# Optimization experiments

Hardware: AMD Instinct MI355X
Metric: run time of the kernel (lower is better)

## Reference

```python
import math
import jax, jax.numpy as jnp
import numpy as np

IN_CH = 512
OUT_CH = 512
KSIZE = 3
STYLE_DIM = 512
EPS = 1e-8


def setup_inputs() -> dict:
    key = jax.random.key(0)
    ks = jax.random.split(key, 8)
    B, H, W = 16, 32, 32
    x = jax.random.normal(ks[0], (B, IN_CH, H, W), dtype=jnp.float32)
    style = jax.random.normal(ks[1], (B, STYLE_DIM), dtype=jnp.float32)
    noise = jax.random.normal(ks[2], (B, 1, 2 * H, 2 * W), dtype=jnp.float32)
    # learned params (matching torch init semantics)
    conv_weight = jax.random.normal(ks[3], (OUT_CH, IN_CH, KSIZE, KSIZE), dtype=jnp.float32)
    mod_weight = jax.random.normal(ks[4], (IN_CH, STYLE_DIM), dtype=jnp.float32)
    mod_bias = jnp.ones((IN_CH,), dtype=jnp.float32)  # bias_init=1
    noise_weight = jax.random.normal(ks[5], (1,), dtype=jnp.float32) * 0.1
    act_bias = jnp.zeros((OUT_CH,), dtype=jnp.float32)
    return {"x": x, "style": style, "noise": noise, "conv_weight": conv_weight,
            "mod_weight": mod_weight, "mod_bias": mod_bias,
            "noise_weight": noise_weight, "act_bias": act_bias}


def _blur_kernel_2d():
    k = jnp.array([1.0, 3.0, 3.0, 1.0], dtype=jnp.float32)
    k2 = k[None, :] * k[:, None]
    k2 = k2 / k2.sum()
    return k2 * 4.0  # upsample_factor**2


def _styled_conv_up(x, style, conv_weight, mod_weight, mod_bias,
                    noise_weight, act_bias, noise):
    B, C_in, H, W = x.shape
    # EqualLinear modulation: scale = 1/sqrt(style_dim), lr_mul=1
    s = style @ (mod_weight * (1.0 / math.sqrt(STYLE_DIM))).T + mod_bias  # [B, C_in]
    # modulate + demodulate per-sample weights
    wscale = 1.0 / math.sqrt(C_in * KSIZE * KSIZE)
    w = wscale * conv_weight[None] * s[:, None, :, None, None]  # [B, out, in, k, k]
    demod = jax.lax.rsqrt(jnp.sum(w * w, axis=(2, 3, 4)) + EPS)  # [B, out]
    w = w * demod[:, :, None, None, None]
    # conv_transpose2d(stride=2, padding=0) == lhs_dilated conv with spatially
    # flipped kernel. torch passes weight as (in, out, k, k); equivalent OIHW
    # forward kernel is flip(w) with layout (out, in, k, k).
    w_flip = jnp.flip(w, axis=(-2, -1))

    def single(xi, wi):  # xi [in,H,W], wi [out,in,k,k]
        return jax.lax.conv_general_dilated(
            xi[None], wi, window_strides=(1, 1),
            padding=[(KSIZE - 1, KSIZE - 1)] * 2,
            lhs_dilation=(2, 2),
            dimension_numbers=("NCHW", "OIHW", "NCHW"))[0]

    out = jax.vmap(single)(x, w_flip)  # [B, out, 2H+1, 2W+1] for k=3
    # Blur: upfirdn2d(kernel=4x4, pad=(1,1)) -> depthwise valid conv
    Bc, Co, Ho, Wo = out.shape
    kb = _blur_kernel_2d()[None, None]  # [1,1,4,4] (symmetric, flip is a no-op)
    out = jax.lax.conv_general_dilated(
        out.reshape(Bc * Co, 1, Ho, Wo), kb, window_strides=(1, 1),
        padding=[(1, 1), (1, 1)],
        dimension_numbers=("NCHW", "OIHW", "NCHW"))
    out = out.reshape(Bc, Co, Ho + 2 - 3, Wo + 2 - 3)  # [B, out, 2H, 2W]
    # noise injection + FusedLeakyReLU (slope 0.2, scale sqrt(2))
    out = out + noise_weight * noise
    out = jax.nn.leaky_relu(out + act_bias.reshape(1, -1, 1, 1), 0.2) * math.sqrt(2.0)
    return out


def reference(x, style, noise, conv_weight, mod_weight, mod_bias,
              noise_weight, act_bias):
    return _styled_conv_up(x, style, conv_weight, mod_weight, mod_bias,
                           noise_weight, act_bias, noise)
```

## Files before the change

### kernel.cpp

```cpp
#include <hip/hip_runtime.h>
#include <math.h>


typedef __attribute__((ext_vector_type(8))) __bf16 bf16x8;
typedef __attribute__((ext_vector_type(4))) float f32x4;

#define WSCALE 0.014731391274719739f
#define SSCALE 0.044194173824159216f

__device__ __forceinline__ unsigned short f2bf(float f) {
  unsigned u = __builtin_bit_cast(unsigned, f);
  u += 0x7fff + ((u >> 16) & 1);
  return (unsigned short)(u >> 16);
}
__device__ __forceinline__ float bf2f(unsigned short h) {
  unsigned u = ((unsigned)h) << 16;
  return __builtin_bit_cast(float, u);
}

__global__ __launch_bounds__(256) void k_style(
    const float* __restrict__ style, const float* __restrict__ mod_w,
    const float* __restrict__ mod_b, float* __restrict__ s_out) {
  int wid  = (blockIdx.x * 256 + threadIdx.x) >> 6;
  int lane = threadIdx.x & 63;
  int b = wid >> 9, ic = wid & 511;
  float acc = 0.f;
  for (int j = lane; j < 512; j += 64)
    acc += style[b * 512 + j] * mod_w[ic * 512 + j];
  for (int off = 32; off > 0; off >>= 1) acc += __shfl_down(acc, off);
  if (lane == 0) s_out[b * 512 + ic] = acc * SSCALE + mod_b[ic];
}

__device__ const int SLABTAP[9] = {0, 2, 6, 8, 1, 7, 3, 5, 4};
__device__ const int SLABOFF[4] = {0, 4, 6, 8};
__device__ const int TAPN[4]    = {4, 2, 2, 1};
__device__ const int TOFFp[4][4] = {{0,-1,-34,-35},{0,-34,0,0},{0,-1,0,0},{0,0,0,0}};

__global__ __launch_bounds__(256) void k_w2(
    const float* __restrict__ conv_w, unsigned short* __restrict__ W2,
    float* __restrict__ w2s) {
  __shared__ float t[4608];
  const int oc = blockIdx.x;
  for (int i = threadIdx.x; i < 4608; i += 256) t[i] = conv_w[oc * 4608 + i];
  __syncthreads();
  for (int i = threadIdx.x; i < 4608; i += 256) {
    int tg = i >> 9, ic = i & 511;
    W2[((size_t)(tg * 512 + oc)) * 512 + ic] = f2bf(t[ic * 9 + SLABTAP[tg]]);
  }
  for (int i = threadIdx.x; i < 512; i += 256) {
    float a = 0.f;
    #pragma unroll
    for (int tg = 0; tg < 9; tg++) { float w = t[i * 9 + tg]; a += w * w; }
    w2s[oc * 512 + i] = a;
  }
}

__global__ __launch_bounds__(256) void k_demod(
    const float* __restrict__ w2s, const float* __restrict__ s,
    float* __restrict__ dscale) {
  int wid  = (blockIdx.x * 256 + threadIdx.x) >> 6;
  int lane = threadIdx.x & 63;
  int b = wid >> 9, oc = wid & 511;
  float acc = 0.f;
  for (int ic = lane; ic < 512; ic += 64) {
    float sv = s[b * 512 + ic];
    acc += sv * sv * w2s[oc * 512 + ic];
  }
  for (int off = 32; off > 0; off >>= 1) acc += __shfl_down(acc, off);
  if (lane == 0)
    dscale[b * 512 + oc] = WSCALE * rsqrtf(WSCALE * WSCALE * acc + 1e-8f);
}

__global__ __launch_bounds__(256) void k_xs2(
    const float* __restrict__ x, const float* __restrict__ s,
    unsigned short* __restrict__ S2) {
  __shared__ float xt[64][65];
  const int b = blockIdx.z, ic0 = blockIdx.y * 64, r0 = blockIdx.x * 2;
  for (int i = threadIdx.x; i < 4096; i += 256) {
    int icL = i >> 6, pxL = i & 63;
    int gr = r0 + (pxL >> 5), gc = pxL & 31;
    xt[icL][pxL] = x[((b * 512 + ic0 + icL) * 32 + gr) * 32 + gc] * s[b * 512 + ic0 + icL];
  }
  __syncthreads();
  for (int i = threadIdx.x; i < 512; i += 256) {
    int pxL = i >> 3, icO = i & 7;
    unsigned short tmp[8];
    #pragma unroll
    for (int k = 0; k < 8; k++) tmp[k] = f2bf(xt[icO * 8 + k][pxL]);
    int gr = r0 + (pxL >> 5), gc = pxL & 31;
    int R = (gr + 1) * 34 + (gc + 1);
    *(uint4*)(&S2[((size_t)b * 1156 + R) * 512 + ic0 + icO * 8]) = *(const uint4*)tmp;
  }
}

__global__ void k_zero(unsigned short* __restrict__ S2) {
  int b = blockIdx.y, id = blockIdx.x;
  int ry, rx;
  if (id < 34)       { ry = 0;        rx = id; }
  else if (id < 68)  { ry = 33;       rx = id - 34; }
  else if (id < 100) { ry = id - 67;  rx = 0; }
  else               { ry = id - 99;  rx = 33; }
  ((unsigned*)(S2 + ((size_t)b * 1156 + ry * 34 + rx) * 512))[threadIdx.x] = 0;
}

__global__ __launch_bounds__(256, 2) void k_gemm(
    const unsigned short* __restrict__ S2, const unsigned short* __restrict__ W2,
    const float* __restrict__ dscale, unsigned short* __restrict__ I, int b_base) {
  __shared__ __align__(16) unsigned short As[128][64];
  __shared__ __align__(16) unsigned short Bs[256][64];

  const int nblk = gridDim.x, qq = nblk >> 3, lid = blockIdx.x;
  const int swz = (lid & 7) * qq + (lid >> 3);
  const int bl = swz / 80;  int rr = swz - bl * 80;
  const int p  = rr / 20;   rr -= p * 20;
  const int nt = rr >> 2, mt = rr & 3;
  const int b  = b_base + bl;
  const int m0 = mt * 128, n0 = nt * 256;

  const int tid = threadIdx.x, lane = tid & 63;
  const int wv = tid >> 6, wm = wv >> 1, wn = wv & 1;
  const int l15 = lane & 15, quad = lane >> 4;
  const int ntap = TAPN[p], soff = SLABOFF[p];
  const int kq = tid & 7, rw = tid >> 3;

  int gRow[8];
  #pragma unroll
  for (int it = 0; it < 8; it++) {
    int n = n0 + it * 32 + rw;
    if (n < 1089) {
      int uy = n / 33, ux = n - uy * 33;
      gRow[it] = b * 1156 + (uy + 1) * 34 + (ux + 1);
    } else gRow[it] = -1;
  }

  f32x4 acc[4][8];
  #pragma unroll
  for (int m = 0; m < 4; m++)
    #pragma unroll
    for (int n = 0; n < 8; n++) acc[m][n] = (f32x4)0.f;

  const int kend = ntap * 512;

  uint4 ra[4], rb[8];
  {
    const int off0 = TOFFp[p][0];
    #pragma unroll
    for (int it = 0; it < 4; it++)
      ra[it] = *(const uint4*)(W2 + ((size_t)(soff * 512 + m0 + it * 32 + rw)) * 512 + kq * 8);
    #pragma unroll
    for (int it = 0; it < 8; it++) {
      uint4 v = make_uint4(0u, 0u, 0u, 0u);
      if (gRow[it] >= 0)
        v = *(const uint4*)(S2 + (size_t)(gRow[it] + off0) * 512 + kq * 8);
      rb[it] = v;
    }
  }

  #pragma unroll 1
  for (int k0 = 0; k0 < kend; k0 += 64) {
    __syncthreads();
    #pragma unroll
    for (int it = 0; it < 4; it++) {
      int r = it * 32 + rw;
      *(uint4*)(&As[r][(kq ^ (r & 7)) * 8]) = ra[it];
    }
    #pragma unroll
    for (int it = 0; it < 8; it++) {
      int r = it * 32 + rw;
      *(uint4*)(&Bs[r][(kq ^ (r & 7)) * 8]) = rb[it];
    }
    const int k1 = k0 + 64;
    if (k1 < kend) {
      const int tj1   = k1 >> 9;
      const int icw1  = k1 & 511;
      const int off1  = TOFFp[p][tj1];
      const int slab1 = soff + tj1;
      #pragma unroll
      for (int it = 0; it < 4; it++)
        ra[it] = *(const uint4*)(W2 + ((size_t)(slab1 * 512 + m0 + it * 32 + rw)) * 512 + icw1 + kq * 8);
      #pragma unroll
      for (int it = 0; it < 8; it++) {
        uint4 v = make_uint4(0u, 0u, 0u, 0u);
        if (gRow[it] >= 0)
          v = *(const uint4*)(S2 + (size_t)(gRow[it] + off1) * 512 + icw1 + kq * 8);
        rb[it] = v;
      }
    }
    __syncthreads();
    #pragma unroll
    for (int kk = 0; kk < 2; kk++) {
      bf16x8 af[4], bfr[8];
      #pragma unroll
      for (int m = 0; m < 4; m++) {
        int r = wm * 64 + m * 16 + l15;
        af[m] = *(const bf16x8*)(&As[r][((kk * 4 + quad) ^ (r & 7)) * 8]);
      }
      #pragma unroll
      for (int n = 0; n < 8; n++) {
        int r = wn * 128 + n * 16 + l15;
        bfr[n] = *(const bf16x8*)(&Bs[r][((kk * 4 + quad) ^ (r & 7)) * 8]);
      }
      #pragma unroll
      for (int m = 0; m < 4; m++)
        #pragma unroll
        for (int n = 0; n < 8; n++)
          acc[m][n] = __builtin_amdgcn_mfma_f32_16x16x32_bf16(af[m], bfr[n], acc[m][n], 0, 0, 0);
    }
  }

  float dsv[4][4];
  #pragma unroll
  for (int m = 0; m < 4; m++)
    #pragma unroll
    for (int r = 0; r < 4; r++)
      dsv[m][r] = dscale[b * 512 + m0 + wm * 64 + m * 16 + quad * 4 + r];
  const size_t Ibase = ((size_t)(bl * 4 + p) * 512) * 1096;
  #pragma unroll
  for (int n = 0; n < 8; n++) {
    int nf = n0 + wn * 128 + n * 16 + l15;
    if (nf < 1089) {
      #pragma unroll
      for (int m = 0; m < 4; m++) {
        int oc = m0 + wm * 64 + m * 16 + quad * 4;
        #pragma unroll
        for (int r = 0; r < 4; r++)
          I[Ibase + (size_t)(oc + r) * 1096 + nf] = f2bf(acc[m][n][r] * dsv[m][r]);
      }
    }
  }
}

__global__ __launch_bounds__(256) void k_blur(
    const unsigned short* __restrict__ I, const float* __restrict__ noise,
    const float* __restrict__ noise_w, const float* __restrict__ act_b,
    float* __restrict__ out, int b_base) {
  __shared__ __align__(16) unsigned short Ism[4][1096];
  __shared__ float V[64][67];
  const int oc = blockIdx.x, bl = blockIdx.y, b = b_base + bl;
  for (int i = threadIdx.x; i < 548; i += 256) {
    int p = i / 137, w = i - p * 137;
    *(uint4*)(&Ism[p][w * 8]) =
        *(const uint4*)(I + ((size_t)(bl * 4 + p) * 512 + oc) * 1096 + w * 8);
  }
  __syncthreads();
  for (int i = threadIdx.x; i < 2112; i += 256) {
    int r = i / 66, col = i - r * 66;
    int px_ = (col >= 33), ux = col - 33 * px_;
    float v0 = (r >= 1) ? bf2f(Ism[2 + px_][(r - 1) * 33 + ux]) : 0.f;
    float a_ = bf2f(Ism[px_][r * 33 + ux]);
    float b_ = bf2f(Ism[2 + px_][r * 33 + ux]);
    float c_ = bf2f(Ism[px_][(r + 1) * 33 + ux]);
    float d_ = bf2f(Ism[2 + px_][(r + 1) * 33 + ux]);
    V[2 * r][col]     = 0.25f * v0 + 0.75f * a_ + 0.75f * b_ + 0.25f * c_;
    V[2 * r + 1][col] = 0.25f * a_ + 0.75f * b_ + 0.75f * c_ + 0.25f * d_;
  }
  __syncthreads();
  const float nw = noise_w[0], ab = act_b[oc];
  for (int i = threadIdx.x; i < 2048; i += 256) {
    int qy = i >> 5, rx = i & 31;
    float w0 = (rx >= 1) ? V[qy][33 + rx - 1] : 0.f;
    float a_ = V[qy][rx];
    float b_ = V[qy][33 + rx];
    float c_ = V[qy][rx + 1];
    float d_ = V[qy][33 + rx + 1];
    float o0 = 0.25f * w0 + 0.75f * a_ + 0.75f * b_ + 0.25f * c_;
    float o1 = 0.25f * a_ + 0.75f * b_ + 0.75f * c_ + 0.25f * d_;
    const float2 nv = *(const float2*)(noise + b * 4096 + qy * 64 + 2 * rx);
    o0 += nw * nv.x + ab;  o1 += nw * nv.y + ab;
    o0 = (o0 > 0.f ? o0 : 0.2f * o0) * 1.4142135623730951f;
    o1 = (o1 > 0.f ? o1 : 0.2f * o1) * 1.4142135623730951f;
    float2 ov = make_float2(o0, o1);
    *(float2*)(out + (((size_t)b * 512 + oc) * 64 + qy) * 64 + 2 * rx) = ov;
  }
}

extern "C" void kernel_launch(void* const* d_in, const int* in_sizes, int n_in,
                              void* d_out, int out_size, void* d_ws, size_t ws_size,
                              hipStream_t stream) {
  const float* x       = (const float*)d_in[0];
  const float* style   = (const float*)d_in[1];
  const float* noise   = (const float*)d_in[2];
  const float* conv_w  = (const float*)d_in[3];
  const float* mod_w   = (const float*)d_in[4];
  const float* mod_b   = (const float*)d_in[5];
  const float* noise_w = (const float*)d_in[6];
  const float* act_b   = (const float*)d_in[7];
  float* out = (float*)d_out;

  char* ws = (char*)d_ws;
  float*          s_ws = (float*)ws;
  float*          d_sc = (float*)(ws + 32768);
  float*          w2s  = (float*)(ws + 65536);
  unsigned short* S2   = (unsigned short*)(ws + 65536 + 1048576);
  unsigned short* W2   = (unsigned short*)(ws + 65536 + 1048576 + 18939904);
  unsigned short* I    = (unsigned short*)(ws + 65536 + 1048576 + 18939904 + 4718592);
  const size_t fixed = 65536ull + 1048576ull + 18939904ull + 4718592ull;
  const size_t per_b = (size_t)4 * 512 * 1096 * 2;

  int nb = 16;
  if (ws_size < fixed + 16 * per_b) nb = 8;
  if (ws_size < fixed + 8 * per_b)  nb = 4;
  if (ws_size < fixed + 4 * per_b)  nb = 2;
  if (ws_size < fixed + 2 * per_b)  nb = 1;

  k_style<<<2048, 256, 0, stream>>>(style, mod_w, mod_b, s_ws);
  k_w2<<<512, 256, 0, stream>>>(conv_w, W2, w2s);
  k_demod<<<2048, 256, 0, stream>>>(w2s, s_ws, d_sc);
  k_xs2<<<dim3(16, 8, 16), 256, 0, stream>>>(x, s_ws, S2);
  k_zero<<<dim3(132, 16), 256, 0, stream>>>(S2);
  for (int b0 = 0; b0 < 16; b0 += nb) {
    k_gemm<<<nb * 80, 256, 0, stream>>>(S2, W2, d_sc, I, b0);
    k_blur<<<dim3(512, nb), 256, 0, stream>>>(I, noise, noise_w, act_b, out, b0);
  }
}
```

Before: 416.8 us.

## Pack two batches per GEMM N-dimension to cut tile padding waste

The GEMM now concatenates the spatial positions of two batch samples along N, so 2178 columns fill 9 tiles of 256 instead of 2×5 tiles with a mostly empty last tile. This lowers wasted MFMA work and the block count. The intermediate stride grows to 1152, the launch bound asks for 3 blocks per SM, and the blur epilogue now writes float4 with 4 outputs per thread. Demod scales are loaded per element in the epilogue, which adds scattered loads, and the higher occupancy target may force register spills.

```diff
diff --git a/kernel.cpp b/kernel.cpp
--- a/kernel.cpp
+++ b/kernel.cpp
@@ -7,6 +7,7 @@
 
 #define WSCALE 0.014731391274719739f
 #define SSCALE 0.044194173824159216f
+#define ISTRIDE 1152
 
 __device__ __forceinline__ unsigned short f2bf(float f) {
   unsigned u = __builtin_bit_cast(unsigned, f);
@@ -103,19 +104,20 @@
   ((unsigned*)(S2 + ((size_t)b * 1156 + ry * 34 + rx) * 512))[threadIdx.x] = 0;
 }
 
-__global__ __launch_bounds__(256, 2) void k_gemm(
+__global__ __launch_bounds__(256, 3) void k_gemm(
     const unsigned short* __restrict__ S2, const unsigned short* __restrict__ W2,
-    const float* __restrict__ dscale, unsigned short* __restrict__ I, int b_base) {
+    const float* __restrict__ dscale, unsigned short* __restrict__ I,
+    int b_base, int g, int ntiles, int run) {
   __shared__ __align__(16) unsigned short As[128][64];
   __shared__ __align__(16) unsigned short Bs[256][64];
 
   const int nblk = gridDim.x, qq = nblk >> 3, lid = blockIdx.x;
   const int swz = (lid & 7) * qq + (lid >> 3);
-  const int bl = swz / 80;  int rr = swz - bl * 80;
-  const int p  = rr / 20;   rr -= p * 20;
+  const int grp = swz / run;  int rr = swz - grp * run;
+  const int p  = rr / (ntiles << 2);  rr -= p * (ntiles << 2);
   const int nt = rr >> 2, mt = rr & 3;
-  const int b  = b_base + bl;
   const int m0 = mt * 128, n0 = nt * 256;
+  const int Ngrp = g * 1089;
 
   const int tid = threadIdx.x, lane = tid & 63;
   const int wv = tid >> 6, wm = wv >> 1, wn = wv & 1;
@@ -127,9 +129,11 @@
   #pragma unroll
   for (int it = 0; it < 8; it++) {
     int n = n0 + it * 32 + rw;
-    if (n < 1089) {
-      int uy = n / 33, ux = n - uy * 33;
-      gRow[it] = b * 1156 + (uy + 1) * 34 + (ux + 1);
+    if (n < Ngrp) {
+      int bl2 = n / 1089;
+      int u = n - bl2 * 1089;
+      int uy = u / 33, ux = u - uy * 33;
+      gRow[it] = (b_base + grp * g + bl2) * 1156 + (uy + 1) * 34 + (ux + 1);
     } else gRow[it] = -1;
   }
 
@@ -208,23 +212,23 @@
     }
   }
 
-  float dsv[4][4];
-  #pragma unroll
-  for (int m = 0; m < 4; m++)
-    #pragma unroll
-    for (int r = 0; r < 4; r++)
-      dsv[m][r] = dscale[b * 512 + m0 + wm * 64 + m * 16 + quad * 4 + r];
-  const size_t Ibase = ((size_t)(bl * 4 + p) * 512) * 1096;
   #pragma unroll
   for (int n = 0; n < 8; n++) {
     int nf = n0 + wn * 128 + n * 16 + l15;
-    if (nf < 1089) {
+    if (nf < Ngrp) {
+      int bl2 = nf / 1089;
+      int ul  = nf - bl2 * 1089;
+      int blA = grp * g + bl2;
+      int bgl = b_base + blA;
+      const size_t Ibase = ((size_t)(blA * 4 + p) * 512) * ISTRIDE;
       #pragma unroll
       for (int m = 0; m < 4; m++) {
         int oc = m0 + wm * 64 + m * 16 + quad * 4;
         #pragma unroll
-        for (int r = 0; r < 4; r++)
-          I[Ibase + (size_t)(oc + r) * 1096 + nf] = f2bf(acc[m][n][r] * dsv[m][r]);
+        for (int r = 0; r < 4; r++) {
+          float ds = dscale[bgl * 512 + oc + r];
+          I[Ibase + (size_t)(oc + r) * ISTRIDE + ul] = f2bf(acc[m][n][r] * ds);
+        }
       }
     }
   }
@@ -240,7 +244,7 @@
   for (int i = threadIdx.x; i < 548; i += 256) {
     int p = i / 137, w = i - p * 137;
     *(uint4*)(&Ism[p][w * 8]) =
-        *(const uint4*)(I + ((size_t)(bl * 4 + p) * 512 + oc) * 1096 + w * 8);
+        *(const uint4*)(I + ((size_t)(bl * 4 + p) * 512 + oc) * ISTRIDE + w * 8);
   }
   __syncthreads();
   for (int i = threadIdx.x; i < 2112; i += 256) {
@@ -256,21 +260,26 @@
   }
   __syncthreads();
   const float nw = noise_w[0], ab = act_b[oc];
-  for (int i = threadIdx.x; i < 2048; i += 256) {
-    int qy = i >> 5, rx = i & 31;
+  for (int i = threadIdx.x; i < 1024; i += 256) {
+    int qy = i >> 4, r4 = i & 15;
+    int rx = r4 * 2;
+    float vA0 = V[qy][rx],     vB0 = V[qy][33 + rx];
+    float vA1 = V[qy][rx + 1], vB1 = V[qy][33 + rx + 1];
+    float vA2 = V[qy][rx + 2], vB2 = V[qy][33 + rx + 2];
     float w0 = (rx >= 1) ? V[qy][33 + rx - 1] : 0.f;
-    float a_ = V[qy][rx];
-    float b_ = V[qy][33 + rx];
-    float c_ = V[qy][rx + 1];
-    float d_ = V[qy][33 + rx + 1];
-    float o0 = 0.25f * w0 + 0.75f * a_ + 0.75f * b_ + 0.25f * c_;
-    float o1 = 0.25f * a_ + 0.75f * b_ + 0.75f * c_ + 0.25f * d_;
-    const float2 nv = *(const float2*)(noise + b * 4096 + qy * 64 + 2 * rx);
+    float o0 = 0.25f * w0  + 0.75f * vA0 + 0.75f * vB0 + 0.25f * vA1;
+    float o1 = 0.25f * vA0 + 0.75f * vB0 + 0.75f * vA1 + 0.25f * vB1;
+    float o2 = 0.25f * vB0 + 0.75f * vA1 + 0.75f * vB1 + 0.25f * vA2;
+    float o3 = 0.25f * vA1 + 0.75f * vB1 + 0.75f * vA2 + 0.25f * vB2;
+    const float4 nv = *(const float4*)(noise + b * 4096 + qy * 64 + r4 * 4);
     o0 += nw * nv.x + ab;  o1 += nw * nv.y + ab;
+    o2 += nw * nv.z + ab;  o3 += nw * nv.w + ab;
     o0 = (o0 > 0.f ? o0 : 0.2f * o0) * 1.4142135623730951f;
     o1 = (o1 > 0.f ? o1 : 0.2f * o1) * 1.4142135623730951f;
-    float2 ov = make_float2(o0, o1);
-    *(float2*)(out + (((size_t)b * 512 + oc) * 64 + qy) * 64 + 2 * rx) = ov;
+    o2 = (o2 > 0.f ? o2 : 0.2f * o2) * 1.4142135623730951f;
+    o3 = (o3 > 0.f ? o3 : 0.2f * o3) * 1.4142135623730951f;
+    float4 ov = make_float4(o0, o1, o2, o3);
+    *(float4*)(out + (((size_t)b * 512 + oc) * 64 + qy) * 64 + r4 * 4) = ov;
   }
 }
 
@@ -295,7 +304,7 @@
   unsigned short* W2   = (unsigned short*)(ws + 65536 + 1048576 + 18939904);
   unsigned short* I    = (unsigned short*)(ws + 65536 + 1048576 + 18939904 + 4718592);
   const size_t fixed = 65536ull + 1048576ull + 18939904ull + 4718592ull;
-  const size_t per_b = (size_t)4 * 512 * 1096 * 2;
+  const size_t per_b = (size_t)4 * 512 * ISTRIDE * 2;
 
   int nb = 16;
   if (ws_size < fixed + 16 * per_b) nb = 8;
@@ -309,7 +318,11 @@
   k_xs2<<<dim3(16, 8, 16), 256, 0, stream>>>(x, s_ws, S2);
   k_zero<<<dim3(132, 16), 256, 0, stream>>>(S2);
   for (int b0 = 0; b0 < 16; b0 += nb) {
-    k_gemm<<<nb * 80, 256, 0, stream>>>(S2, W2, d_sc, I, b0);
+    int g      = (nb >= 2) ? 2 : 1;
+    int ngrp   = nb / g;
+    int ntiles = (g * 1089 + 255) / 256;
+    int run    = 4 * ntiles * 4;
+    k_gemm<<<ngrp * run, 256, 0, stream>>>(S2, W2, d_sc, I, b0, g, ntiles, run);
     k_blur<<<dim3(512, nb), 256, 0, stream>>>(I, noise, noise_w, act_b, out, b0);
   }
 }
```

New measurement: 853.5 us. 105% more time.
